# Kernel tuning notes

Measured on AMD Instinct MI355X. Metric: run time of the kernel, lower is better.

The kernel has to match this reference:

```python
import jax, jax.numpy as jnp
import numpy as np
import math

B, S, IN, H, M = 4, 2048, 256, 128, 128  # mem_dim must equal hidden_size


def _xavier(key, shape):
    fan_in, fan_out = shape[0], shape[-1]
    lim = math.sqrt(6.0 / (fan_in + fan_out))
    return jax.random.uniform(key, shape, jnp.float32, -lim, lim)


def setup_inputs() -> dict:
    key = jax.random.key(0)
    ks = jax.random.split(key, 8)
    return dict(
        x=jax.random.normal(ks[0], (B, S, IN), jnp.float32),
        c0=jnp.zeros((M, M), jnp.float32),   # init_hidden matrix memory
        n0=jnp.zeros((M, 1), jnp.float32),   # init_hidden normalizer
        w_q=_xavier(ks[1], (IN, H)), b_q=jnp.zeros((H,), jnp.float32),
        w_k=_xavier(ks[2], (IN, M)), b_k=jnp.zeros((M,), jnp.float32),
        w_v=_xavier(ks[3], (IN, M)), b_v=jnp.zeros((M,), jnp.float32),
        w_i=_xavier(ks[4], (IN, 1)), b_i=jnp.zeros((1,), jnp.float32),
        w_f=_xavier(ks[5], (IN, 1)), b_f=jnp.zeros((1,), jnp.float32),
        w_o=_xavier(ks[6], (IN, H)), b_o=jnp.zeros((H,), jnp.float32),
    )


def reference(x, c0, n0, w_q, b_q, w_k, b_k, w_v, b_v, w_i, b_i, w_f, b_f, w_o, b_o):
    Bb, Ss, Ii = x.shape
    Mm = w_k.shape[1]
    Hh = w_q.shape[1]
    xf = x.reshape(Bb * Ss, Ii)                                  # [N, IN]
    q = xf @ w_q + b_q                                           # [N, H]
    k = (xf @ w_k + b_k) * (1.0 / math.sqrt(Mm))                 # [N, M]
    v = xf @ w_v + b_v                                           # [N, M]
    i_t = jnp.exp(xf @ w_i + b_i)                                # [N, 1]
    f_t = jax.nn.sigmoid(xf @ w_f + b_f)                         # [N, 1]
    # Original loop never updates c_prev: c_t[n] = f[n]*c0 + i[n]*outer(v[n], k[n])
    c = f_t[:, :, None] * c0[None] + i_t[:, :, None] * (v[:, :, None] * k[:, None, :])  # [N, M, M]
    n = f_t[:, :, None] * n0[None] + i_t[:, :, None] * k[:, :, None]                    # [N, M, 1]
    c = c.reshape(Bb, Ss, Mm, Mm)
    n = n.reshape(Bb, Ss, Mm, 1)
    q4 = q.reshape(Bb, Ss, Hh)
    nq = jnp.einsum('bsm,bsm->bs', n[..., 0], q4)                # n^T q
    denom = jnp.maximum(jnp.abs(nq), 1.0)[..., None]             # max(|n^T q|, 1)
    h_tilde = jnp.einsum('bsmk,bsk->bsm', c, q4) / denom         # (c_t q) / denom
    o = jax.nn.sigmoid(xf @ w_o + b_o).reshape(Bb, Ss, Hh)
    h = o * h_tilde                                              # [B, S, H]
    return (h, c, n)
```

## Files before the change

### kernel.cpp

```cpp
#include <hip/hip_runtime.h>
#include <math.h>

#define B_    4
#define S_    2048
#define IN_   256
#define H_    128
#define M_    128
#define NROWS (B_ * S_)
#define RPB   16
#define GRP   4
#define NGRP  4
#define TPB   512
#define XPAD  260

typedef float f4_t __attribute__((ext_vector_type(4)));

__global__ __launch_bounds__(TPB) void xlstm_pipe(
    const float* __restrict__ x,
    const float* __restrict__ c0,
    const float* __restrict__ n0,
    const float* __restrict__ w_q, const float* __restrict__ b_q,
    const float* __restrict__ w_k, const float* __restrict__ b_k,
    const float* __restrict__ w_v, const float* __restrict__ b_v,
    const float* __restrict__ w_i, const float* __restrict__ b_i,
    const float* __restrict__ w_f, const float* __restrict__ b_f,
    const float* __restrict__ w_o, const float* __restrict__ b_o,
    float* __restrict__ out_h,
    float* __restrict__ out_c,
    float* __restrict__ out_n)
{
    __shared__ float xs[RPB][XPAD];
    __shared__ float bq[2][GRP][M_];
    __shared__ float bk[2][GRP][M_];
    __shared__ float bv[2][GRP][M_];
    __shared__ float bo[2][GRP][M_];
    __shared__ float itf[RPB][2];
    __shared__ float scalb[2][GRP][2];

    const int t    = threadIdx.x;
    const int row0 = blockIdx.x * RPB;
    const bool prod = (t < 256);

    for (int p4 = t; p4 < RPB * IN_ / 4; p4 += TPB) {
        int p = p4 * 4;
        float4 v = *(const float4*)(x + (size_t)row0 * IN_ + p);
        *(float4*)&xs[p >> 8][p & 255] = v;
    }
    __syncthreads();

    const int cg  = t & 31;
    const int mat = (t >> 5) & 3;
    const int rh  = (t >> 7) & 1;
    const int c4  = cg * 4;
    const int col = t & 127;
    const float* W    = (mat==0)? w_q : (mat==1)? w_k : (mat==2)? w_v : w_o;
    const float* BIAS = (mat==0)? b_q : (mat==1)? b_k : (mat==2)? b_v : b_o;
    const f4_t bias4 = *(const f4_t*)(BIAS + c4);
    const float kscale = 0.08838834764831843f;

    const int ct   = t & 255;
    const int base = ct * 4;
    const int jj   = base & 127;

    float c0qA = 0.f, c0qB = 0.f;

    #pragma unroll 1
    for (int s = 0; s <= NGRP; ++s) {
        if (prod) {
            if (s == 0) {
                const int gr = t >> 4, gseg = t & 15;
                const float* xrow = &xs[gr][gseg * 16];
                float pi = 0.f, pf = 0.f;
                #pragma unroll
                for (int u = 0; u < 4; ++u) {
                    float4 xv  = *(const float4*)(xrow + u * 4);
                    float4 wiv = *(const float4*)(w_i + gseg * 16 + u * 4);
                    float4 wfv = *(const float4*)(w_f + gseg * 16 + u * 4);
                    pi = fmaf(xv.x,wiv.x, fmaf(xv.y,wiv.y, fmaf(xv.z,wiv.z, fmaf(xv.w,wiv.w, pi))));
                    pf = fmaf(xv.x,wfv.x, fmaf(xv.y,wfv.y, fmaf(xv.z,wfv.z, fmaf(xv.w,wfv.w, pf))));
                }
                #pragma unroll
                for (int mm = 1; mm < 16; mm <<= 1) { pi += __shfl_xor(pi, mm); pf += __shfl_xor(pf, mm); }
                if (gseg == 0) {
                    itf[gr][0] = __expf(pi + b_i[0]);
                    itf[gr][1] = 1.f / (1.f + __expf(-(pf + b_f[0])));
                }
            }
            if (s > 0) {
                const int b = (s - 1) & 1;
                #pragma unroll
                for (int rr = 0; rr < 2; ++rr) {
                    const int lrow = rh * 2 + rr;
                    const int row  = (s - 1) * GRP + lrow;
                    const size_t grow = (size_t)(row0 + row);
                    const float iv = itf[row][0], fv = itf[row][1];
                    out_n[grow * M_ + col] = fmaf(fv, n0[col], iv * bk[b][lrow][col]);
                    const float kq  = scalb[b][lrow][0];
                    const float n0q = scalb[b][lrow][1];
                    const float nq = fmaf(fv, n0q, iv * kq);
                    const float denom = fmaxf(fabsf(nq), 1.f);
                    const float c0q = rr ? c0qB : c0qA;
                    const float ht = fmaf(fv, c0q, iv * bv[b][lrow][col] * kq) / denom;
                    out_h[grow * H_ + col] = bo[b][lrow][col] * ht;
                }
            }
            if (s < NGRP) {
                const int b  = s & 1;
                const int r0 = s * GRP + rh * 2;
                f4_t acc0 = (f4_t){0.f,0.f,0.f,0.f};
                f4_t acc1 = (f4_t){0.f,0.f,0.f,0.f};
                #pragma unroll 4
                for (int it = 0; it < 64; ++it) {
                    const int k0 = it * 4;
                    const float* wp = W + (size_t)k0 * H_ + c4;
                    f4_t w0 = *(const f4_t*)(wp);
                    f4_t w1 = *(const f4_t*)(wp + H_);
                    f4_t w2 = *(const f4_t*)(wp + 2 * H_);
                    f4_t w3 = *(const f4_t*)(wp + 3 * H_);
                    f4_t xv0 = *(const f4_t*)&xs[r0][k0];
                    f4_t xv1 = *(const f4_t*)&xs[r0 + 1][k0];
                    acc0 += xv0.x*w0 + xv0.y*w1 + xv0.z*w2 + xv0.w*w3;
                    acc1 += xv1.x*w0 + xv1.y*w1 + xv1.z*w2 + xv1.w*w3;
                }
                acc0 += bias4; acc1 += bias4;
                if (mat == 1) { acc0 *= kscale; acc1 *= kscale; }
                if (mat == 3) {
                    acc0.x = 1.f/(1.f+__expf(-acc0.x)); acc0.y = 1.f/(1.f+__expf(-acc0.y));
                    acc0.z = 1.f/(1.f+__expf(-acc0.z)); acc0.w = 1.f/(1.f+__expf(-acc0.w));
                    acc1.x = 1.f/(1.f+__expf(-acc1.x)); acc1.y = 1.f/(1.f+__expf(-acc1.y));
                    acc1.z = 1.f/(1.f+__expf(-acc1.z)); acc1.w = 1.f/(1.f+__expf(-acc1.w));
                }
                float (*DST)[M_] = (mat==0)? bq[b] : (mat==1)? bk[b] : (mat==2)? bv[b] : bo[b];
                const int lr = rh * 2;
                *(f4_t*)&DST[lr][c4]     = acc0;
                *(f4_t*)&DST[lr + 1][c4] = acc1;
            }
        } else if (s > 0) {
            const int b     = (s - 1) & 1;
            const int gbase = (s - 1) * GRP;
            f4_t k40 = *(const f4_t*)&bk[b][0][jj];
            f4_t k41 = *(const f4_t*)&bk[b][1][jj];
            const float if0 = itf[gbase][0],     ff0 = itf[gbase][1];
            const float if1 = itf[gbase + 1][0], ff1 = itf[gbase + 1][1];
            float* o0 = out_c + (size_t)(row0 + gbase)     * (M_ * M_);
            float* o1 = out_c + (size_t)(row0 + gbase + 1) * (M_ * M_);
            #pragma unroll 2
            for (int ch = 0; ch < 12; ++ch) {
                const int p = (ch << 10) + base;
                const int m = p >> 7;
                f4_t c0v = *(const f4_t*)(c0 + p);
                f4_t oa = ff0 * c0v + (if0 * bv[b][0][m]) * k40;
                f4_t ob = ff1 * c0v + (if1 * bv[b][1][m]) * k41;
                __builtin_nontemporal_store(oa, (f4_t*)(o0 + p));
                __builtin_nontemporal_store(ob, (f4_t*)(o1 + p));
            }
        }
        __syncthreads();
        if (prod) {
            if (s < NGRP) {
                const int b  = s & 1;
                const int lr = rh * 2;
                float a0 = 0.f, a1 = 0.f;
                const float* c0row = c0 + (size_t)col * M_;
                #pragma unroll 2
                for (int j4 = 0; j4 < M_; j4 += 4) {
                    f4_t w4 = *(const f4_t*)(c0row + j4);
                    f4_t qa = *(const f4_t*)&bq[b][lr][j4];
                    f4_t qb = *(const f4_t*)&bq[b][lr + 1][j4];
                    a0 = fmaf(w4.x,qa.x, fmaf(w4.y,qa.y, fmaf(w4.z,qa.z, fmaf(w4.w,qa.w, a0))));
                    a1 = fmaf(w4.x,qb.x, fmaf(w4.y,qb.y, fmaf(w4.z,qb.z, fmaf(w4.w,qb.w, a1))));
                }
                c0qA = a0; c0qB = a1;
                const int wv = t >> 6;
                const int l  = t & 63;
                const float ka  = bk[b][wv][l], kb2 = bk[b][wv][l + 64];
                const float qa2 = bq[b][wv][l], qb2 = bq[b][wv][l + 64];
                float pkq = fmaf(ka, qa2, kb2 * qb2);
                float pnq = fmaf(n0[l], qa2, n0[l + 64] * qb2);
                #pragma unroll
                for (int mm = 1; mm < 64; mm <<= 1) { pkq += __shfl_xor(pkq, mm); pnq += __shfl_xor(pnq, mm); }
                if (l == 0) { scalb[b][wv][0] = pkq; scalb[b][wv][1] = pnq; }

                const int gbase = s * GRP;
                #pragma unroll
                for (int ch = 12; ch < 16; ++ch) {
                    const int p = (ch << 10) + base;
                    const int m = p >> 7;
                    f4_t c0v = *(const f4_t*)(c0 + p);
                    #pragma unroll
                    for (int r = 0; r < GRP; ++r) {
                        f4_t k4 = *(const f4_t*)&bk[b][r][jj];
                        float sf = itf[gbase + r][0] * bv[b][r][m];
                        f4_t o4 = itf[gbase + r][1] * c0v + sf * k4;
                        __builtin_nontemporal_store(o4,
                            (f4_t*)(out_c + (size_t)(row0 + gbase + r) * (M_ * M_) + p));
                    }
                }
            }
        } else if (s > 0) {
            const int b     = (s - 1) & 1;
            const int gbase = (s - 1) * GRP;
            f4_t k42 = *(const f4_t*)&bk[b][2][jj];
            f4_t k43 = *(const f4_t*)&bk[b][3][jj];
            const float if2 = itf[gbase + 2][0], ff2 = itf[gbase + 2][1];
            const float if3 = itf[gbase + 3][0], ff3 = itf[gbase + 3][1];
            float* o2 = out_c + (size_t)(row0 + gbase + 2) * (M_ * M_);
            float* o3 = out_c + (size_t)(row0 + gbase + 3) * (M_ * M_);
            #pragma unroll 2
            for (int ch = 0; ch < 12; ++ch) {
                const int p = (ch << 10) + base;
                const int m = p >> 7;
                f4_t c0v = *(const f4_t*)(c0 + p);
                f4_t oa = ff2 * c0v + (if2 * bv[b][2][m]) * k42;
                f4_t ob = ff3 * c0v + (if3 * bv[b][3][m]) * k43;
                __builtin_nontemporal_store(oa, (f4_t*)(o2 + p));
                __builtin_nontemporal_store(ob, (f4_t*)(o3 + p));
            }
        }
        __syncthreads();
    }
}

extern "C" void kernel_launch(void* const* d_in, const int* in_sizes, int n_in,
                              void* d_out, int out_size, void* d_ws, size_t ws_size,
                              hipStream_t stream) {
    const float* x   = (const float*)d_in[0];
    const float* c0  = (const float*)d_in[1];
    const float* n0  = (const float*)d_in[2];
    const float* w_q = (const float*)d_in[3];  const float* b_q = (const float*)d_in[4];
    const float* w_k = (const float*)d_in[5];  const float* b_k = (const float*)d_in[6];
    const float* w_v = (const float*)d_in[7];  const float* b_v = (const float*)d_in[8];
    const float* w_i = (const float*)d_in[9];  const float* b_i = (const float*)d_in[10];
    const float* w_f = (const float*)d_in[11]; const float* b_f = (const float*)d_in[12];
    const float* w_o = (const float*)d_in[13]; const float* b_o = (const float*)d_in[14];

    float* out   = (float*)d_out;
    float* out_h = out;
    float* out_c = out + (size_t)NROWS * H_;
    float* out_n = out_c + (size_t)NROWS * M_ * M_;

    hipLaunchKernelGGL(xlstm_pipe, dim3(NROWS / RPB), dim3(TPB), 0, stream,
                       x, c0, n0, w_q, b_q, w_k, b_k, w_v, b_v,
                       w_i, b_i, w_f, b_f, w_o, b_o,
                       out_h, out_c, out_n);
}
```

Before: 144.2 us.

## Stage c0 in padded LDS, double rows per block, rebalance c-tile stores

Doubles rows per block to 32 and stages the whole c0 matrix into padded dynamic shared memory, so the c-tile writes and the c0·q dot products read c0 from LDS instead of global memory. The i/f gate computation moves into a prologue for all rows. The consumer warps now write all 16 chunks of each c row, and the producer's leftover chunk writes are dropped. Nontemporal stores become plain stores. The trade-off is heavy LDS use (about 66 KB extra), which limits the CU to one block, and the grid is halved to 256 blocks. This may leave the write-bound output stream with too little parallelism, and the change in cache behaviour from dropping nontemporal stores is uncertain.

New measurement: 188.8 us. +31.0%, slower.

```diff
diff --git a/kernel.cpp b/kernel.cpp
--- a/kernel.cpp
+++ b/kernel.cpp
@@ -7,11 +7,13 @@
 #define H_    128
 #define M_    128
 #define NROWS (B_ * S_)
-#define RPB   16
+#define RPB   32
 #define GRP   4
-#define NGRP  4
+#define NGRP  8
 #define TPB   512
 #define XPAD  260
+#define C0STRIDE 130
+#define C0BYTES  (128 * C0STRIDE * 4)
 
 typedef float f4_t __attribute__((ext_vector_type(4)));
 
@@ -36,6 +38,7 @@
     __shared__ float bo[2][GRP][M_];
     __shared__ float itf[RPB][2];
     __shared__ float scalb[2][GRP][2];
+    extern __shared__ float c0s[];
 
     const int t    = threadIdx.x;
     const int row0 = blockIdx.x * RPB;
@@ -45,6 +48,32 @@
         int p = p4 * 4;
         float4 v = *(const float4*)(x + (size_t)row0 * IN_ + p);
         *(float4*)&xs[p >> 8][p & 255] = v;
+    }
+    for (int i = t; i < 4096; i += TPB) {
+        f4_t v = *(const f4_t*)(c0 + (size_t)i * 4);
+        int m = i >> 5, j4 = i & 31;
+        *(f4_t*)&c0s[m * C0STRIDE + j4 * 4] = v;
+    }
+    __syncthreads();
+
+    {
+        const int gr = t >> 4, gseg = t & 15;
+        const float* xrow = &xs[gr][gseg * 16];
+        float pi = 0.f, pf = 0.f;
+        #pragma unroll
+        for (int u = 0; u < 4; ++u) {
+            float4 xv  = *(const float4*)(xrow + u * 4);
+            float4 wiv = *(const float4*)(w_i + gseg * 16 + u * 4);
+            float4 wfv = *(const float4*)(w_f + gseg * 16 + u * 4);
+            pi = fmaf(xv.x,wiv.x, fmaf(xv.y,wiv.y, fmaf(xv.z,wiv.z, fmaf(xv.w,wiv.w, pi))));
+            pf = fmaf(xv.x,wfv.x, fmaf(xv.y,wfv.y, fmaf(xv.z,wfv.z, fmaf(xv.w,wfv.w, pf))));
+        }
+        #pragma unroll
+        for (int mm = 1; mm < 16; mm <<= 1) { pi += __shfl_xor(pi, mm); pf += __shfl_xor(pf, mm); }
+        if (gseg == 0) {
+            itf[gr][0] = __expf(pi + b_i[0]);
+            itf[gr][1] = 1.f / (1.f + __expf(-(pf + b_f[0])));
+        }
     }
     __syncthreads();
 
@@ -55,7 +84,7 @@
     const int col = t & 127;
     const float* W    = (mat==0)? w_q : (mat==1)? w_k : (mat==2)? w_v : w_o;
     const float* BIAS = (mat==0)? b_q : (mat==1)? b_k : (mat==2)? b_v : b_o;
-    const f4_t bias4 = *(const f4_t*)(BIAS + c4);
+    const f4_t bias4 = prod ? *(const f4_t*)(BIAS + c4) : (f4_t){0,0,0,0};
     const float kscale = 0.08838834764831843f;
 
     const int ct   = t & 255;
@@ -67,25 +96,6 @@
     #pragma unroll 1
     for (int s = 0; s <= NGRP; ++s) {
         if (prod) {
-            if (s == 0) {
-                const int gr = t >> 4, gseg = t & 15;
-                const float* xrow = &xs[gr][gseg * 16];
-                float pi = 0.f, pf = 0.f;
-                #pragma unroll
-                for (int u = 0; u < 4; ++u) {
-                    float4 xv  = *(const float4*)(xrow + u * 4);
-                    float4 wiv = *(const float4*)(w_i + gseg * 16 + u * 4);
-                    float4 wfv = *(const float4*)(w_f + gseg * 16 + u * 4);
-                    pi = fmaf(xv.x,wiv.x, fmaf(xv.y,wiv.y, fmaf(xv.z,wiv.z, fmaf(xv.w,wiv.w, pi))));
-                    pf = fmaf(xv.x,wfv.x, fmaf(xv.y,wfv.y, fmaf(xv.z,wfv.z, fmaf(xv.w,wfv.w, pf))));
-                }
-                #pragma unroll
-                for (int mm = 1; mm < 16; mm <<= 1) { pi += __shfl_xor(pi, mm); pf += __shfl_xor(pf, mm); }
-                if (gseg == 0) {
-                    itf[gr][0] = __expf(pi + b_i[0]);
-                    itf[gr][1] = 1.f / (1.f + __expf(-(pf + b_f[0])));
-                }
-            }
             if (s > 0) {
                 const int b = (s - 1) & 1;
                 #pragma unroll
@@ -145,14 +155,14 @@
             float* o0 = out_c + (size_t)(row0 + gbase)     * (M_ * M_);
             float* o1 = out_c + (size_t)(row0 + gbase + 1) * (M_ * M_);
             #pragma unroll 2
-            for (int ch = 0; ch < 12; ++ch) {
+            for (int ch = 0; ch < 16; ++ch) {
                 const int p = (ch << 10) + base;
                 const int m = p >> 7;
-                f4_t c0v = *(const f4_t*)(c0 + p);
+                f4_t c0v = *(const f4_t*)&c0s[m * C0STRIDE + (p & 127)];
                 f4_t oa = ff0 * c0v + (if0 * bv[b][0][m]) * k40;
                 f4_t ob = ff1 * c0v + (if1 * bv[b][1][m]) * k41;
-                __builtin_nontemporal_store(oa, (f4_t*)(o0 + p));
-                __builtin_nontemporal_store(ob, (f4_t*)(o1 + p));
+                *(f4_t*)(o0 + p) = oa;
+                *(f4_t*)(o1 + p) = ob;
             }
         }
         __syncthreads();
@@ -161,7 +171,7 @@
                 const int b  = s & 1;
                 const int lr = rh * 2;
                 float a0 = 0.f, a1 = 0.f;
-                const float* c0row = c0 + (size_t)col * M_;
+                const float* c0row = c0s + (size_t)col * C0STRIDE;
                 #pragma unroll 2
                 for (int j4 = 0; j4 < M_; j4 += 4) {
                     f4_t w4 = *(const f4_t*)(c0row + j4);
@@ -180,22 +190,6 @@
                 #pragma unroll
                 for (int mm = 1; mm < 64; mm <<= 1) { pkq += __shfl_xor(pkq, mm); pnq += __shfl_xor(pnq, mm); }
                 if (l == 0) { scalb[b][wv][0] = pkq; scalb[b][wv][1] = pnq; }
-
-                const int gbase = s * GRP;
-                #pragma unroll
-                for (int ch = 12; ch < 16; ++ch) {
-                    const int p = (ch << 10) + base;
-                    const int m = p >> 7;
-                    f4_t c0v = *(const f4_t*)(c0 + p);
-                    #pragma unroll
-                    for (int r = 0; r < GRP; ++r) {
-                        f4_t k4 = *(const f4_t*)&bk[b][r][jj];
-                        float sf = itf[gbase + r][0] * bv[b][r][m];
-                        f4_t o4 = itf[gbase + r][1] * c0v + sf * k4;
-                        __builtin_nontemporal_store(o4,
-                            (f4_t*)(out_c + (size_t)(row0 + gbase + r) * (M_ * M_) + p));
-                    }
-                }
             }
         } else if (s > 0) {
             const int b     = (s - 1) & 1;
@@ -207,14 +201,14 @@
             float* o2 = out_c + (size_t)(row0 + gbase + 2) * (M_ * M_);
             float* o3 = out_c + (size_t)(row0 + gbase + 3) * (M_ * M_);
             #pragma unroll 2
-            for (int ch = 0; ch < 12; ++ch) {
+            for (int ch = 0; ch < 16; ++ch) {
                 const int p = (ch << 10) + base;
                 const int m = p >> 7;
-                f4_t c0v = *(const f4_t*)(c0 + p);
+                f4_t c0v = *(const f4_t*)&c0s[m * C0STRIDE + (p & 127)];
                 f4_t oa = ff2 * c0v + (if2 * bv[b][2][m]) * k42;
                 f4_t ob = ff3 * c0v + (if3 * bv[b][3][m]) * k43;
-                __builtin_nontemporal_store(oa, (f4_t*)(o2 + p));
-                __builtin_nontemporal_store(ob, (f4_t*)(o3 + p));
+                *(f4_t*)(o2 + p) = oa;
+                *(f4_t*)(o3 + p) = ob;
             }
         }
         __syncthreads();
@@ -239,7 +233,11 @@
     float* out_c = out + (size_t)NROWS * H_;
     float* out_n = out_c + (size_t)NROWS * M_ * M_;
 
-    hipLaunchKernelGGL(xlstm_pipe, dim3(NROWS / RPB), dim3(TPB), 0, stream,
+    (void)hipFuncSetAttribute((const void*)xlstm_pipe,
+                              hipFuncAttributeMaxDynamicSharedMemorySize,
+                              C0BYTES);
+
+    hipLaunchKernelGGL(xlstm_pipe, dim3(NROWS / RPB), dim3(TPB), C0BYTES, stream,
                        x, c0, n0, w_q, b_q, w_k, b_k, w_v, b_v,
                        w_i, b_i, w_f, b_f, w_o, b_o,
                        out_h, out_c, out_n);
```
